# Performance work log

Measured on AMD Instinct MI355X. Metric: run time of the kernel, lower is better.

The kernel has to match this reference:

```python
import jax, jax.numpy as jnp
import numpy as np
from jax.ops import segment_sum, segment_max

N, E = 50000, 800000
IN_FEATS, H, D_HID, N_CLASSES = 256, 4, 32, 47
NEG_SLOPE = 0.2


def leaky_relu(x, slope=NEG_SLOPE):
    return jnp.where(x >= 0, x, slope * x)


def gat_conv(h, W, attn_l, attn_r, src, dst, n_nodes, heads, d_out):
    # h: [N, F_in]; W: [F_in, heads*d_out]; attn_l/attn_r: [heads, d_out]
    feat = (h @ W).reshape(n_nodes, heads, d_out)          # [N, H, D]
    el = jnp.sum(feat * attn_l, axis=-1)                   # [N, H]
    er = jnp.sum(feat * attn_r, axis=-1)                   # [N, H]
    e = leaky_relu(el[src] + er[dst])                      # [E, H]
    # segment softmax over incoming edges of each dst node
    e_max = segment_max(e, dst, num_segments=n_nodes)      # [N, H]
    e_exp = jnp.exp(e - e_max[dst])                        # [E, H]
    denom = segment_sum(e_exp, dst, num_segments=n_nodes)  # [N, H]
    alpha = e_exp / denom[dst]                             # [E, H]
    msg = feat[src] * alpha[..., None]                     # [E, H, D]
    return segment_sum(msg, dst, num_segments=n_nodes)     # [N, H, D]


def setup_inputs() -> dict:
    key = jax.random.key(0)
    ks = jax.random.split(key, 12)
    hd = H * D_HID
    def glorot(k, shape):
        fan = shape[0] + shape[-1] if len(shape) == 2 else int(np.prod(shape))
        return jax.random.normal(k, shape, dtype=jnp.float32) * np.sqrt(2.0 / fan)
    return {
        "x": jax.random.normal(ks[0], (N, IN_FEATS), dtype=jnp.float32),
        "src": jax.random.randint(ks[1], (E,), 0, N),
        "dst": jax.random.randint(ks[2], (E,), 0, N),
        "W1": glorot(ks[3], (IN_FEATS, hd)),
        "al1": glorot(ks[4], (H, D_HID)),
        "ar1": glorot(ks[5], (H, D_HID)),
        "W2": glorot(ks[6], (hd, hd)),
        "al2": glorot(ks[7], (H, D_HID)),
        "ar2": glorot(ks[8], (H, D_HID)),
        "W3": glorot(ks[9], (hd, H * N_CLASSES)),
        "al3": glorot(ks[10], (H, N_CLASSES)),
        "ar3": glorot(ks[11], (H, N_CLASSES)),
    }


def reference(x, src, dst, W1, al1, ar1, W2, al2, ar2, W3, al3, ar3):
    # layer 1: ELU activation, flatten heads
    h = gat_conv(x, W1, al1, ar1, src, dst, N, H, D_HID)
    h = jax.nn.elu(h).reshape(N, H * D_HID)
    # layer 2
    h = gat_conv(h, W2, al2, ar2, src, dst, N, H, D_HID)
    h = jax.nn.elu(h).reshape(N, H * D_HID)
    # layer 3: no activation, mean over heads, log softmax
    h = gat_conv(h, W3, al3, ar3, src, dst, N, H, N_CLASSES)
    h = h.mean(axis=1)                                      # [N, n_classes]
    return jax.nn.log_softmax(h, axis=-1)
```

## Files before the change

kernel.cpp:

```cpp
#include <hip/hip_runtime.h>
#include <hip/hip_bf16.h>
#include <math.h>
#include <string.h>

#define N_NODES 50000
#define N_EDGES 800000
#define NH 4
#define LSTR 68

typedef unsigned int u32;
typedef unsigned short u16;
typedef __attribute__((ext_vector_type(8))) short bf16x8;
typedef __attribute__((ext_vector_type(4))) float f32x4;
typedef __attribute__((ext_vector_type(2))) float f32x2;

__device__ __forceinline__ u32 pack_bf2(float a, float b) {
    __hip_bfloat162 h2 = __float22bfloat162_rn(make_float2(a, b));
    u32 r;
    memcpy(&r, &h2, 4);
    return r;
}
__device__ __forceinline__ f32x2 bf2_to_v2(u32 u) {
    f32x2 v;
    v.x = __uint_as_float(u << 16);
    v.y = __uint_as_float(u & 0xffff0000u);
    return v;
}
__device__ __forceinline__ short bf16r(float f) {
    __hip_bfloat16 h = __float2bfloat16(f);
    short s;
    memcpy(&s, &h, 2);
    return s;
}
__device__ __forceinline__ void pkfma_lo(f32x2& acc, f32x2 a, f32x2 b) {
    asm("v_pk_fma_f32 %0, %1, %2, %0 op_sel:[0,0,0] op_sel_hi:[0,1,1]"
        : "+v"(acc) : "v"(a), "v"(b));
}
__device__ __forceinline__ void pkfma_hi(f32x2& acc, f32x2 a, f32x2 b) {
    asm("v_pk_fma_f32 %0, %1, %2, %0 op_sel:[1,0,0] op_sel_hi:[1,1,1]"
        : "+v"(acc) : "v"(a), "v"(b));
}

__device__ __forceinline__ float wred_max(float v) {
#pragma unroll
    for (int o = 32; o > 0; o >>= 1) v = fmaxf(v, __shfl_xor(v, o));
    return v;
}
__device__ __forceinline__ float wred_sum(float v) {
#pragma unroll
    for (int o = 32; o > 0; o >>= 1) v += __shfl_xor(v, o);
    return v;
}


__global__ void k_hist(const int* __restrict__ dst, int* __restrict__ deg) {
    int i = blockIdx.x * 256 + threadIdx.x;
    if (i < N_EDGES) atomicAdd(&deg[dst[i]], 1);
}

__global__ __launch_bounds__(1024) void k_scan1(const int* __restrict__ deg,
                                                int* __restrict__ offs,
                                                int* __restrict__ bsum) {
    __shared__ int tmp[1024];
    int b = blockIdx.x, t = threadIdx.x;
    int i = b * 1024 + t;
    int v = (i < N_NODES) ? deg[i] : 0;
    tmp[t] = v;
    __syncthreads();
    for (int off = 1; off < 1024; off <<= 1) {
        int add = (t >= off) ? tmp[t - off] : 0;
        __syncthreads();
        tmp[t] += add;
        __syncthreads();
    }
    if (i < N_NODES) offs[i] = tmp[t] - v;
    if (t == 1023) bsum[b] = tmp[t];
}

__global__ void k_scan2(int* __restrict__ bsum, int nb) {
    int t = threadIdx.x & 63;
    int v = (t < nb) ? bsum[t] : 0;
    int orig = v;
#pragma unroll
    for (int o = 1; o < 64; o <<= 1) {
        int u = __shfl_up(v, o);
        if (t >= o) v += u;
    }
    if (t < nb) bsum[t] = v - orig;
}

__global__ __launch_bounds__(1024) void k_scan3(int* __restrict__ offs,
                                                const int* __restrict__ bsum,
                                                int* __restrict__ cursor) {
    int b = blockIdx.x, t = threadIdx.x;
    int i = b * 1024 + t;
    if (i < N_NODES) {
        int o = offs[i] + bsum[b];
        offs[i] = o;
        cursor[i] = o;
    }
    if (b == 0 && t == 0) offs[N_NODES] = N_EDGES;
}

__global__ void k_scatter(const int* __restrict__ src, const int* __restrict__ dst,
                          int* __restrict__ cursor, int* __restrict__ csrc) {
    int i = blockIdx.x * 256 + threadIdx.x;
    if (i < N_EDGES) {
        int p = atomicAdd(&cursor[dst[i]], 1);
        csrc[p] = src[i];
    }
}

__device__ __forceinline__ u16 pack_elem(const float* W, int i, int K, int NT, int NOUT) {
    int j = i & 7;
    int lane = (i >> 3) & 63;
    int rest = i >> 9;
    int nt = rest % NT;
    int kt = rest / NT;
    int k = kt * 32 + (lane >> 4) * 8 + j;
    int col = nt * 16 + (lane & 15);
    float v = (col < NOUT) ? W[(size_t)k * NOUT + col] : 0.f;
    return (u16)bf16r(v);
}
__device__ __forceinline__ u16 pack_elem3(const float* W, int i) {
    int j = i & 7;
    int lane = (i >> 3) & 63;
    int rest = i >> 9;
    int nt = rest % 12;
    int kt = rest / 12;
    int k = kt * 32 + (lane >> 4) * 8 + j;
    int col = nt * 16 + (lane & 15);
    int h = col / 48, d = col % 48;
    float v = (d < 47) ? W[(size_t)k * 188 + h * 47 + d] : 0.f;
    return (u16)bf16r(v);
}
__global__ void prep_all(const float* __restrict__ W1, const float* __restrict__ W2,
                         const float* __restrict__ W3, u16* __restrict__ wp1,
                         u16* __restrict__ wp2, u16* __restrict__ wp3) {
    int idx = blockIdx.x * 256 + threadIdx.x;
    if (idx < 32768) {
        wp1[idx] = pack_elem(W1, idx, 256, 8, 128);
    } else if (idx < 49152) {
        int i = idx - 32768;
        wp2[i] = pack_elem(W2, i, 128, 8, 128);
    } else if (idx < 73728) {
        int i = idx - 49152;
        wp3[i] = pack_elem3(W3, i);
    }
}

template <int K, int NOUT, int NP, bool AF32, bool DOTS, bool HEADPAD>
__global__ __launch_bounds__(256) void gemm_mfma(const void* __restrict__ Av,
                                                 const u16* __restrict__ Wp,
                                                 u16* __restrict__ feat,
                                                 const float* __restrict__ al,
                                                 const float* __restrict__ ar,
                                                 float* __restrict__ el,
                                                 float* __restrict__ er) {
    constexpr int NT = NP / 16;
    constexpr int KT = K / 32;
    int w = threadIdx.x >> 6, l = threadIdx.x & 63;
    int tile_m0 = blockIdx.x * 64 + w * 16;
    int c15 = l & 15;
    int rowA = tile_m0 + c15;
    if (rowA >= N_NODES) rowA = N_NODES - 1;
    int g = l >> 4;

    f32x4 acc[NT];
#pragma unroll
    for (int nt = 0; nt < NT; ++nt) acc[nt] = (f32x4){0.f, 0.f, 0.f, 0.f};

    for (int kt = 0; kt < KT; ++kt) {
        bf16x8 a;
        if constexpr (AF32) {
            const float* ap = (const float*)Av + (size_t)rowA * K + kt * 32 + g * 8;
            float4 f0 = *reinterpret_cast<const float4*>(ap);
            float4 f1 = *reinterpret_cast<const float4*>(ap + 4);
            a[0] = bf16r(f0.x); a[1] = bf16r(f0.y); a[2] = bf16r(f0.z); a[3] = bf16r(f0.w);
            a[4] = bf16r(f1.x); a[5] = bf16r(f1.y); a[6] = bf16r(f1.z); a[7] = bf16r(f1.w);
        } else {
            a = *reinterpret_cast<const bf16x8*>((const u16*)Av + (size_t)rowA * K + kt * 32 + g * 8);
        }
        const u16* wp = Wp + ((size_t)kt * NT) * 512 + (size_t)l * 8;
#pragma unroll
        for (int nt = 0; nt < NT; ++nt) {
            bf16x8 b = *reinterpret_cast<const bf16x8*>(wp + nt * 512);
            acc[nt] = __builtin_amdgcn_mfma_f32_16x16x32_bf16(a, b, acc[nt], 0, 0, 0);
        }
    }

    int rowD0 = tile_m0 + g * 4;
#pragma unroll
    for (int nt = 0; nt < NT; ++nt) {
        int col = nt * 16 + c15;
#pragma unroll
        for (int r = 0; r < 4; ++r) {
            int row = rowD0 + r;
            if (row < N_NODES)
                feat[(size_t)row * NP + col] = (u16)bf16r(acc[nt][r]);
        }
    }

    if constexpr (DOTS) {
        float alv[NT], arv[NT];
#pragma unroll
        for (int nt = 0; nt < NT; ++nt) {
            if constexpr (HEADPAD) {
                int h = nt / 3, m = nt % 3;
                if (m == 2) {
                    alv[nt] = (c15 < 15) ? al[h * 47 + 32 + c15] : 0.f;
                    arv[nt] = (c15 < 15) ? ar[h * 47 + 32 + c15] : 0.f;
                } else {
                    alv[nt] = al[h * 47 + m * 16 + c15];
                    arv[nt] = ar[h * 47 + m * 16 + c15];
                }
            } else {
                alv[nt] = al[nt * 16 + c15];
                arv[nt] = ar[nt * 16 + c15];
            }
        }
#pragma unroll
        for (int r = 0; r < 4; ++r) {
            float hlv[NH] = {0.f, 0.f, 0.f, 0.f};
            float hrv[NH] = {0.f, 0.f, 0.f, 0.f};
#pragma unroll
            for (int nt = 0; nt < NT; ++nt) {
                constexpr int NTH = NT / NH;
                int h = nt / NTH;
                hlv[h] = fmaf(acc[nt][r], alv[nt], hlv[h]);
                hrv[h] = fmaf(acc[nt][r], arv[nt], hrv[h]);
            }
#pragma unroll
            for (int o = 1; o < 16; o <<= 1) {
#pragma unroll
                for (int j = 0; j < NH; ++j) {
                    hlv[j] += __shfl_xor(hlv[j], o);
                    hrv[j] += __shfl_xor(hrv[j], o);
                }
            }
            int row = rowD0 + r;
            if (c15 == 0 && row < N_NODES) {
                *reinterpret_cast<float4*>(el + (size_t)row * NH) =
                    make_float4(hlv[0], hlv[1], hlv[2], hlv[3]);
                *reinterpret_cast<float4*>(er + (size_t)row * NH) =
                    make_float4(hrv[0], hrv[1], hrv[2], hrv[3]);
            }
        }
    }
}

__device__ __forceinline__ void alpha_chunk_T(const float* __restrict__ el,
                                              const int* __restrict__ csrc,
                                              float4 erv, int base, int i1, u32 rowb,
                                              float4 mref, float4 vinv, bool online,
                                              float* __restrict__ lalT,
                                              u32* __restrict__ loff, int lane) {
    int e = base + lane;
    bool act = e < i1;
    int srcn = act ? csrc[e] : 0;
    float4 elv = make_float4(0.f, 0.f, 0.f, 0.f);
    if (act) elv = *reinterpret_cast<const float4*>(el + (size_t)srcn * NH);
    float e0 = elv.x + erv.x; e0 = e0 >= 0.f ? e0 : 0.2f * e0;
    float e1 = elv.y + erv.y; e1 = e1 >= 0.f ? e1 : 0.2f * e1;
    float e2 = elv.z + erv.z; e2 = e2 >= 0.f ? e2 : 0.2f * e2;
    float e3 = elv.w + erv.w; e3 = e3 >= 0.f ? e3 : 0.2f * e3;
    float4 a4;
    if (online) {
        const float NEG = -__builtin_inff();
        float f0 = act ? e0 : NEG, f1 = act ? e1 : NEG, f2 = act ? e2 : NEG, f3 = act ? e3 : NEG;
        float m0 = wred_max(f0), m1 = wred_max(f1), m2 = wred_max(f2), m3 = wred_max(f3);
        float p0 = act ? __expf(e0 - m0) : 0.f;
        float p1 = act ? __expf(e1 - m1) : 0.f;
        float p2 = act ? __expf(e2 - m2) : 0.f;
        float p3 = act ? __expf(e3 - m3) : 0.f;
        float s0 = wred_sum(p0), s1 = wred_sum(p1), s2 = wred_sum(p2), s3 = wred_sum(p3);
        a4 = make_float4(act ? p0 / s0 : 0.f, act ? p1 / s1 : 0.f,
                         act ? p2 / s2 : 0.f, act ? p3 / s3 : 0.f);
    } else {
        a4 = make_float4(act ? __expf(e0 - mref.x) * vinv.x : 0.f,
                         act ? __expf(e1 - mref.y) * vinv.y : 0.f,
                         act ? __expf(e2 - mref.z) * vinv.z : 0.f,
                         act ? __expf(e3 - mref.w) * vinv.w : 0.f);
    }
    lalT[0 * LSTR + lane] = a4.x;
    lalT[1 * LSTR + lane] = a4.y;
    lalT[2 * LSTR + lane] = a4.z;
    lalT[3 * LSTR + lane] = a4.w;
    loff[lane] = (u32)srcn * rowb;
}

__device__ __forceinline__ void stats_pass(const float* __restrict__ el,
                                           const int* __restrict__ csrc,
                                           float4 erv, int i0, int i1, int lane,
                                           float4& mout, float4& vout) {
    const float NEG = -__builtin_inff();
    float m0 = NEG, m1 = NEG, m2 = NEG, m3 = NEG;
    float s0 = 0.f, s1 = 0.f, s2 = 0.f, s3 = 0.f;
    for (int base = i0; base < i1; base += 64) {
        int i = base + lane;
        bool act = i < i1;
        int srcn = act ? csrc[i] : 0;
        float4 elv = make_float4(0.f, 0.f, 0.f, 0.f);
        if (act) elv = *reinterpret_cast<const float4*>(el + (size_t)srcn * NH);
        float e0 = elv.x + erv.x; e0 = e0 >= 0.f ? e0 : 0.2f * e0;
        float e1 = elv.y + erv.y; e1 = e1 >= 0.f ? e1 : 0.2f * e1;
        float e2 = elv.z + erv.z; e2 = e2 >= 0.f ? e2 : 0.2f * e2;
        float e3 = elv.w + erv.w; e3 = e3 >= 0.f ? e3 : 0.2f * e3;
        if (!act) { e0 = NEG; e1 = NEG; e2 = NEG; e3 = NEG; }
        float c0 = wred_max(e0), c1 = wred_max(e1), c2 = wred_max(e2), c3 = wred_max(e3);
        float nm0 = fmaxf(m0, c0), nm1 = fmaxf(m1, c1), nm2 = fmaxf(m2, c2), nm3 = fmaxf(m3, c3);
        float p0 = act ? __expf(e0 - nm0) : 0.f;
        float p1 = act ? __expf(e1 - nm1) : 0.f;
        float p2 = act ? __expf(e2 - nm2) : 0.f;
        float p3 = act ? __expf(e3 - nm3) : 0.f;
        float S0 = wred_sum(p0), S1 = wred_sum(p1), S2 = wred_sum(p2), S3 = wred_sum(p3);
        s0 = s0 * __expf(m0 - nm0) + S0; m0 = nm0;
        s1 = s1 * __expf(m1 - nm1) + S1; m1 = nm1;
        s2 = s2 * __expf(m2 - nm2) + S2; m2 = nm2;
        s3 = s3 * __expf(m3 - nm3) + S3; m3 = nm3;
    }
    mout = make_float4(m0, m1, m2, m3);
    vout = make_float4(1.f / s0, 1.f / s1, 1.f / s2, 1.f / s3);
}

__global__ __launch_bounds__(256) void gat_agg128(const u16* __restrict__ feat,
                                                  const float* __restrict__ el,
                                                  const float* __restrict__ er,
                                                  const int* __restrict__ offs,
                                                  const int* __restrict__ csrc,
                                                  u16* __restrict__ out) {
    __shared__ float lalT[4][4][LSTR];
    __shared__ u32 loff[4][64];
    int wave = threadIdx.x >> 6;
    int lane = threadIdx.x & 63;
    int n = blockIdx.x * 4 + wave;
    int sub = lane >> 4, sl = lane & 15;
    int h = sl >> 2;
    u32 soff = (u32)sl * 16u;
    int i0 = offs[n], i1 = offs[n + 1];
    int d = i1 - i0;
    f32x2 acc0 = (f32x2){0.f, 0.f}, acc1 = acc0, acc2 = acc0, acc3 = acc0;
    if (d > 0) {
        float4 erv = *reinterpret_cast<const float4*>(er + (size_t)n * NH);
        float4 mref = make_float4(0.f, 0.f, 0.f, 0.f), vinv = mref;
        bool onechunk = d <= 64;
        if (!onechunk) stats_pass(el, csrc, erv, i0, i1, lane, mref, vinv);
        const char* fbase = (const char*)feat;
        for (int base = i0; base < i1; base += 64) {
            alpha_chunk_T(el, csrc, erv, base, i1, 256u, mref, vinv, onechunk,
                          &lalT[wave][0][0], &loff[wave][0], lane);
            int cnt = i1 - base; if (cnt > 64) cnt = 64;
            int cpad = (cnt + 7) & ~7;
            for (int j = 0; j < cpad; j += 8) {
                u32 o0 = loff[wave][j + sub] + soff;
                u32 o1 = loff[wave][j + 4 + sub] + soff;
                uint4 q0 = *reinterpret_cast<const uint4*>(fbase + o0);
                uint4 q1 = *reinterpret_cast<const uint4*>(fbase + o1);
                f32x2 ap = (f32x2){lalT[wave][h][j + sub], lalT[wave][h][j + 4 + sub]};
                pkfma_lo(acc0, ap, bf2_to_v2(q0.x));
                pkfma_lo(acc1, ap, bf2_to_v2(q0.y));
                pkfma_lo(acc2, ap, bf2_to_v2(q0.z));
                pkfma_lo(acc3, ap, bf2_to_v2(q0.w));
                pkfma_hi(acc0, ap, bf2_to_v2(q1.x));
                pkfma_hi(acc1, ap, bf2_to_v2(q1.y));
                pkfma_hi(acc2, ap, bf2_to_v2(q1.z));
                pkfma_hi(acc3, ap, bf2_to_v2(q1.w));
            }
        }
    }
    float v[8] = {acc0.x, acc0.y, acc1.x, acc1.y, acc2.x, acc2.y, acc3.x, acc3.y};
#pragma unroll
    for (int k = 0; k < 8; ++k) {
        v[k] += __shfl_xor(v[k], 16);
        v[k] += __shfl_xor(v[k], 32);
    }
    if (sub == 0) {
        float o[8];
#pragma unroll
        for (int k = 0; k < 8; ++k) o[k] = v[k] > 0.f ? v[k] : expm1f(v[k]);
        uint4 wv = make_uint4(pack_bf2(o[0], o[1]), pack_bf2(o[2], o[3]),
                              pack_bf2(o[4], o[5]), pack_bf2(o[6], o[7]));
        *reinterpret_cast<uint4*>(out + (size_t)n * 128 + sl * 8) = wv;
    }
}

__global__ __launch_bounds__(256) void gat_agg_final(const u16* __restrict__ feat,
                                                     const float* __restrict__ el,
                                                     const float* __restrict__ er,
                                                     const int* __restrict__ offs,
                                                     const int* __restrict__ csrc,
                                                     float* __restrict__ out) {
    __shared__ float lalT[4][4][LSTR];
    __shared__ u32 loff[4][64];
    __shared__ float lds[4][192];
    int wave = threadIdx.x >> 6;
    int lane = threadIdx.x & 63;
    int n = blockIdx.x * 4 + wave;
    int sub = lane >> 5, sl = lane & 31;
    bool act = sl < 24;
    int h = act ? (sl / 6) : 0;
    u32 soff = (u32)sl * 16u;
    int i0 = offs[n], i1 = offs[n + 1];
    int d = i1 - i0;
    f32x2 acc0 = (f32x2){0.f, 0.f}, acc1 = acc0, acc2 = acc0, acc3 = acc0;
    if (d > 0) {
        float4 erv = *reinterpret_cast<const float4*>(er + (size_t)n * NH);
        float4 mref = make_float4(0.f, 0.f, 0.f, 0.f), vinv = mref;
        bool onechunk = d <= 64;
        if (!onechunk) stats_pass(el, csrc, erv, i0, i1, lane, mref, vinv);
        const char* fbase = (const char*)feat;
        for (int base = i0; base < i1; base += 64) {
            alpha_chunk_T(el, csrc, erv, base, i1, 384u, mref, vinv, onechunk,
                          &lalT[wave][0][0], &loff[wave][0], lane);
            int cnt = i1 - base; if (cnt > 64) cnt = 64;
            int cpad = (cnt + 3) & ~3;
            if (act) {
                for (int j = 0; j < cpad; j += 4) {
                    u32 o0 = loff[wave][j + sub] + soff;
                    u32 o1 = loff[wave][j + 2 + sub] + soff;
                    uint4 q0 = *reinterpret_cast<const uint4*>(fbase + o0);
                    uint4 q1 = *reinterpret_cast<const uint4*>(fbase + o1);
                    f32x2 ap = (f32x2){lalT[wave][h][j + sub], lalT[wave][h][j + 2 + sub]};
                    pkfma_lo(acc0, ap, bf2_to_v2(q0.x));
                    pkfma_lo(acc1, ap, bf2_to_v2(q0.y));
                    pkfma_lo(acc2, ap, bf2_to_v2(q0.z));
                    pkfma_lo(acc3, ap, bf2_to_v2(q0.w));
                    pkfma_hi(acc0, ap, bf2_to_v2(q1.x));
                    pkfma_hi(acc1, ap, bf2_to_v2(q1.y));
                    pkfma_hi(acc2, ap, bf2_to_v2(q1.z));
                    pkfma_hi(acc3, ap, bf2_to_v2(q1.w));
                }
            }
        }
    }
    float v[8] = {acc0.x, acc0.y, acc1.x, acc1.y, acc2.x, acc2.y, acc3.x, acc3.y};
#pragma unroll
    for (int k = 0; k < 8; ++k) v[k] += __shfl_xor(v[k], 32);
    if (sub == 0 && act) {
        float4 lo = make_float4(v[0], v[1], v[2], v[3]);
        float4 hi = make_float4(v[4], v[5], v[6], v[7]);
        *reinterpret_cast<float4*>(&lds[wave][sl * 8]) = lo;
        *reinterpret_cast<float4*>(&lds[wave][sl * 8 + 4]) = hi;
    }
    __syncthreads();
    float u = (lane < 47)
                  ? 0.25f * (lds[wave][lane] + lds[wave][48 + lane] +
                             lds[wave][96 + lane] + lds[wave][144 + lane])
                  : -__builtin_inff();
    float mx = u;
#pragma unroll
    for (int o = 32; o > 0; o >>= 1) mx = fmaxf(mx, __shfl_xor(mx, o));
    float ex = (lane < 47) ? __expf(u - mx) : 0.f;
    float sm = ex;
#pragma unroll
    for (int o = 32; o > 0; o >>= 1) sm += __shfl_xor(sm, o);
    if (lane < 47) out[(size_t)n * 47 + lane] = u - mx - logf(sm);
}


extern "C" void kernel_launch(void* const* d_in, const int* in_sizes, int n_in,
                              void* d_out, int out_size, void* d_ws, size_t ws_size,
                              hipStream_t stream) {
    const float* x = (const float*)d_in[0];
    const int* src = (const int*)d_in[1];
    const int* dst = (const int*)d_in[2];
    const float* W1 = (const float*)d_in[3];
    const float* al1 = (const float*)d_in[4];
    const float* ar1 = (const float*)d_in[5];
    const float* W2 = (const float*)d_in[6];
    const float* al2 = (const float*)d_in[7];
    const float* ar2 = (const float*)d_in[8];
    const float* W3 = (const float*)d_in[9];
    const float* al3 = (const float*)d_in[10];
    const float* ar3 = (const float*)d_in[11];
    float* out = (float*)d_out;

    char* p = (char*)d_ws;
    auto alloc = [&](size_t bytes) {
        char* r = p;
        p += (bytes + 255) & ~(size_t)255;
        return r;
    };
    u16* bufA = (u16*)alloc((size_t)N_NODES * 128 * 2);
    u16* bufC = (u16*)alloc((size_t)N_NODES * 128 * 2);
    u16* featb = (u16*)alloc((size_t)N_NODES * 192 * 2);
    float* el = (float*)alloc((size_t)N_NODES * NH * 4);
    float* er = (float*)alloc((size_t)N_NODES * NH * 4);
    u16* wp1 = (u16*)alloc((size_t)32768 * 2);
    u16* wp2 = (u16*)alloc((size_t)16384 * 2);
    u16* wp3 = (u16*)alloc((size_t)24576 * 2);
    int* deg = (int*)alloc((size_t)N_NODES * 4);
    int* offs = (int*)alloc((size_t)(N_NODES + 1) * 4);
    int* cursor = (int*)alloc((size_t)N_NODES * 4);
    int* bsum = (int*)alloc(64 * 4);
    int* csrc = (int*)alloc((size_t)N_EDGES * 4);

    prep_all<<<288, 256, 0, stream>>>(W1, W2, W3, wp1, wp2, wp3);

    hipMemsetAsync(deg, 0, (size_t)N_NODES * 4, stream);
    k_hist<<<(N_EDGES + 255) / 256, 256, 0, stream>>>(dst, deg);
    k_scan1<<<49, 1024, 0, stream>>>(deg, offs, bsum);
    k_scan2<<<1, 64, 0, stream>>>(bsum, 49);
    k_scan3<<<49, 1024, 0, stream>>>(offs, bsum, cursor);
    k_scatter<<<(N_EDGES + 255) / 256, 256, 0, stream>>>(src, dst, cursor, csrc);

    int gemm_grid = (N_NODES + 63) / 64;
    gemm_mfma<256, 128, 128, true, true, false><<<gemm_grid, 256, 0, stream>>>(x, wp1, featb, al1, ar1, el, er);
    gat_agg128<<<N_NODES / 4, 256, 0, stream>>>(featb, el, er, offs, csrc, bufA);
    gemm_mfma<128, 128, 128, false, true, false><<<gemm_grid, 256, 0, stream>>>(bufA, wp2, featb, al2, ar2, el, er);
    gat_agg128<<<N_NODES / 4, 256, 0, stream>>>(featb, el, er, offs, csrc, bufC);
    gemm_mfma<128, 192, 192, false, true, true><<<gemm_grid, 256, 0, stream>>>(bufC, wp3, featb, al3, ar3, el, er);
    gat_agg_final<<<N_NODES / 4, 256, 0, stream>>>(featb, el, er, offs, csrc, out);
}
```

Measured before the change: 298.3 us.

## Remap 128-wide aggregation lanes to features and fold scan2 into scan3

The 128-feature aggregation kernel is remapped so that each lane owns two contiguous feature columns and walks every edge. It issues four 4-byte gathers per group of four edges and reads offsets and alphas as vector LDS loads. This replaces four edge-subgroups doing 16-byte gathers, which then needed a cross-subgroup shuffle reduction. The mapping drops the final shuffle reduction and lets every lane write its output, at the cost of more, smaller global loads per edge. Separately, the single-block scan2 kernel is removed: each scan3 block now computes its own prefix from the block sums with a wave reduction, saving one launch.

Measured after the change: 294.7 us. About the same (-1.2%).

```diff
diff --git a/kernel.cpp b/kernel.cpp
--- a/kernel.cpp
+++ b/kernel.cpp
@@ -47,6 +47,11 @@
     return v;
 }
 __device__ __forceinline__ float wred_sum(float v) {
+#pragma unroll
+    for (int o = 32; o > 0; o >>= 1) v += __shfl_xor(v, o);
+    return v;
+}
+__device__ __forceinline__ int wred_sum_i(int v) {
 #pragma unroll
     for (int o = 32; o > 0; o >>= 1) v += __shfl_xor(v, o);
     return v;
@@ -77,25 +82,20 @@
     if (t == 1023) bsum[b] = tmp[t];
 }
 
-__global__ void k_scan2(int* __restrict__ bsum, int nb) {
-    int t = threadIdx.x & 63;
-    int v = (t < nb) ? bsum[t] : 0;
-    int orig = v;
-#pragma unroll
-    for (int o = 1; o < 64; o <<= 1) {
-        int u = __shfl_up(v, o);
-        if (t >= o) v += u;
-    }
-    if (t < nb) bsum[t] = v - orig;
-}
-
 __global__ __launch_bounds__(1024) void k_scan3(int* __restrict__ offs,
                                                 const int* __restrict__ bsum,
-                                                int* __restrict__ cursor) {
+                                                int* __restrict__ cursor, int nb) {
+    __shared__ int pfx;
     int b = blockIdx.x, t = threadIdx.x;
+    if (t < 64) {
+        int v = (t < nb && t < b) ? bsum[t] : 0;
+        v = wred_sum_i(v);
+        if (t == 0) pfx = v;
+    }
+    __syncthreads();
     int i = b * 1024 + t;
     if (i < N_NODES) {
-        int o = offs[i] + bsum[b];
+        int o = offs[i] + pfx;
         offs[i] = o;
         cursor[i] = o;
     }
@@ -334,12 +334,11 @@
     int wave = threadIdx.x >> 6;
     int lane = threadIdx.x & 63;
     int n = blockIdx.x * 4 + wave;
-    int sub = lane >> 4, sl = lane & 15;
-    int h = sl >> 2;
-    u32 soff = (u32)sl * 16u;
+    int h = lane >> 4;
+    u32 lo4 = (u32)lane * 4u;
     int i0 = offs[n], i1 = offs[n + 1];
     int d = i1 - i0;
-    f32x2 acc0 = (f32x2){0.f, 0.f}, acc1 = acc0, acc2 = acc0, acc3 = acc0;
+    f32x2 acc = (f32x2){0.f, 0.f};
     if (d > 0) {
         float4 erv = *reinterpret_cast<const float4*>(er + (size_t)n * NH);
         float4 mref = make_float4(0.f, 0.f, 0.f, 0.f), vinv = mref;
@@ -350,38 +349,26 @@
             alpha_chunk_T(el, csrc, erv, base, i1, 256u, mref, vinv, onechunk,
                           &lalT[wave][0][0], &loff[wave][0], lane);
             int cnt = i1 - base; if (cnt > 64) cnt = 64;
-            int cpad = (cnt + 7) & ~7;
-            for (int j = 0; j < cpad; j += 8) {
-                u32 o0 = loff[wave][j + sub] + soff;
-                u32 o1 = loff[wave][j + 4 + sub] + soff;
-                uint4 q0 = *reinterpret_cast<const uint4*>(fbase + o0);
-                uint4 q1 = *reinterpret_cast<const uint4*>(fbase + o1);
-                f32x2 ap = (f32x2){lalT[wave][h][j + sub], lalT[wave][h][j + 4 + sub]};
-                pkfma_lo(acc0, ap, bf2_to_v2(q0.x));
-                pkfma_lo(acc1, ap, bf2_to_v2(q0.y));
-                pkfma_lo(acc2, ap, bf2_to_v2(q0.z));
-                pkfma_lo(acc3, ap, bf2_to_v2(q0.w));
-                pkfma_hi(acc0, ap, bf2_to_v2(q1.x));
-                pkfma_hi(acc1, ap, bf2_to_v2(q1.y));
-                pkfma_hi(acc2, ap, bf2_to_v2(q1.z));
-                pkfma_hi(acc3, ap, bf2_to_v2(q1.w));
+            int cpad = (cnt + 3) & ~3;
+            for (int j = 0; j < cpad; j += 4) {
+                uint4 ov = *reinterpret_cast<const uint4*>(&loff[wave][j]);
+                float4 aq = *reinterpret_cast<const float4*>(&lalT[wave][h][j]);
+                f32x2 aqLo = (f32x2){aq.x, aq.y};
+                f32x2 aqHi = (f32x2){aq.z, aq.w};
+                u32 q0 = *reinterpret_cast<const u32*>(fbase + (ov.x + lo4));
+                u32 q1 = *reinterpret_cast<const u32*>(fbase + (ov.y + lo4));
+                u32 q2 = *reinterpret_cast<const u32*>(fbase + (ov.z + lo4));
+                u32 q3 = *reinterpret_cast<const u32*>(fbase + (ov.w + lo4));
+                pkfma_lo(acc, aqLo, bf2_to_v2(q0));
+                pkfma_hi(acc, aqLo, bf2_to_v2(q1));
+                pkfma_lo(acc, aqHi, bf2_to_v2(q2));
+                pkfma_hi(acc, aqHi, bf2_to_v2(q3));
             }
         }
     }
-    float v[8] = {acc0.x, acc0.y, acc1.x, acc1.y, acc2.x, acc2.y, acc3.x, acc3.y};
-#pragma unroll
-    for (int k = 0; k < 8; ++k) {
-        v[k] += __shfl_xor(v[k], 16);
-        v[k] += __shfl_xor(v[k], 32);
-    }
-    if (sub == 0) {
-        float o[8];
-#pragma unroll
-        for (int k = 0; k < 8; ++k) o[k] = v[k] > 0.f ? v[k] : expm1f(v[k]);
-        uint4 wv = make_uint4(pack_bf2(o[0], o[1]), pack_bf2(o[2], o[3]),
-                              pack_bf2(o[4], o[5]), pack_bf2(o[6], o[7]));
-        *reinterpret_cast<uint4*>(out + (size_t)n * 128 + sl * 8) = wv;
-    }
+    float ox = acc.x > 0.f ? acc.x : expm1f(acc.x);
+    float oy = acc.y > 0.f ? acc.y : expm1f(acc.y);
+    *reinterpret_cast<u32*>(out + (size_t)n * 128 + 2 * lane) = pack_bf2(ox, oy);
 }
 
 __global__ __launch_bounds__(256) void gat_agg_final(const u16* __restrict__ feat,
@@ -500,8 +487,7 @@
     hipMemsetAsync(deg, 0, (size_t)N_NODES * 4, stream);
     k_hist<<<(N_EDGES + 255) / 256, 256, 0, stream>>>(dst, deg);
     k_scan1<<<49, 1024, 0, stream>>>(deg, offs, bsum);
-    k_scan2<<<1, 64, 0, stream>>>(bsum, 49);
-    k_scan3<<<49, 1024, 0, stream>>>(offs, bsum, cursor);
+    k_scan3<<<49, 1024, 0, stream>>>(offs, bsum, cursor, 49);
     k_scatter<<<(N_EDGES + 255) / 256, 256, 0, stream>>>(src, dst, cursor, csrc);
 
     int gemm_grid = (N_NODES + 63) / 64;
```
